# Kernel tuning notes

Measured on AMD Instinct MI355X. Metric: run time of the kernel, lower is better.

Reference implementation:

```python
import math
import jax, jax.numpy as jnp
import numpy as np

B, T, D = 2048, 50, 256
NEG = -100000.0

def setup_inputs() -> dict:
    key = jax.random.key(0)
    ks = jax.random.split(key, 9)
    return {
        "x": jax.random.normal(ks[0], (B, T, D), dtype=jnp.float32),
        "mask": jax.random.randint(ks[1], (B, T, 1), 0, 2, dtype=jnp.int32),
        "time_decay": jax.random.uniform(ks[2], (B, T, 1), dtype=jnp.float32),
        "Wq": jax.random.normal(ks[3], (D, D), dtype=jnp.float32) * (1.0 / math.sqrt(D)),
        "bq": jax.random.normal(ks[4], (D,), dtype=jnp.float32) * 0.01,
        "Wk": jax.random.normal(ks[5], (D, D), dtype=jnp.float32) * (1.0 / math.sqrt(D)),
        "bk": jax.random.normal(ks[6], (D,), dtype=jnp.float32) * 0.01,
        "Wv": jax.random.normal(ks[7], (D, D), dtype=jnp.float32) * (1.0 / math.sqrt(D)),
        "bv": jax.random.normal(ks[8], (D,), dtype=jnp.float32) * 0.01,
    }

def reference(x, mask, time_decay, Wq, bq, Wk, bk, Wv, bv):
    # PositionalEncoding.forward: elementwise multiply by time-decay (broadcast over d_model)
    x = x * time_decay  # [B,T,D]
    q = jnp.einsum('btd,ed->bte', x, Wq) + bq
    k = jnp.einsum('btd,ed->bte', x, Wk) + bk
    v = jnp.einsum('btd,ed->bte', x, Wv) + bv
    # unusual Q/K-side masking (masked_fill before the matmul)
    keep = mask != 0  # [B,T,1]
    q = jnp.where(keep, q, NEG)
    k = jnp.where(keep, k, NEG)
    score = jnp.einsum('btd,bsd->bts', q, k) / math.sqrt(D)  # [B,T,T]
    score = jax.nn.softmax(score, axis=-1)
    # dropout is identity in eval mode
    out = jnp.einsum('bts,bsd->btd', score, v)  # [B,T,D]
    return out[:, -1, :]  # [B,D]
```

## Files before the change

kernel.cpp:

```cpp
#include <hip/hip_runtime.h>


namespace {
constexpr int kB = 2048;
constexpr int kT = 50;
constexpr int kD = 256;
constexpr double kNeg = -100000.0;
constexpr int oM2 = 0;
constexpr int oWvp = 65536;
constexpr int oV0 = 131072;
constexpr int oC = 131328;
constexpr int oW1 = 131584;
constexpr int oW2 = 131840;
constexpr int oDbl = 132096;
}

__global__ __launch_bounds__(256) void precomp(
    const float* __restrict__ Wq, const float* __restrict__ bq,
    const float* __restrict__ Wk, const float* __restrict__ bk,
    const float* __restrict__ Wv, float* __restrict__ ws) {
  const int t = threadIdx.x;
  const int wave = t >> 6;
  const int lane = t & 63;
  const int blk = blockIdx.x;
  __shared__ float coefL[kD];
  __shared__ double red[3][4];

  if (blk < 256) {
    const int a = blk;
    coefL[t] = Wq[(size_t)t * kD + a];
    __syncthreads();
    const float* kcol = Wk + t;
    float pre[8];
#pragma unroll
    for (int k = 0; k < 8; ++k) pre[k] = kcol[(size_t)k * kD];
    float acc = 0.f;
    for (int j0 = 0; j0 < kD; j0 += 8) {
      float cur[8];
#pragma unroll
      for (int k = 0; k < 8; ++k) cur[k] = pre[k];
      const int nx = (j0 + 8 < kD) ? (j0 + 8) : 0;
#pragma unroll
      for (int k = 0; k < 8; ++k) pre[k] = kcol[(size_t)(nx + k) * kD];
#pragma unroll
      for (int k = 0; k < 8; ++k) acc += coefL[j0 + k] * cur[k];
    }
    ws[oM2 + (a >> 2) * 1024 + 4 * t + (a & 3)] = acc;
  } else if (blk < 258) {
    const float* W = (blk == 256) ? Wk : Wq;
    const float* coef = (blk == 256) ? bq : bk;
    coefL[t] = coef[t];
    __syncthreads();
    const float* col = W + t;
    float pre[8];
#pragma unroll
    for (int k = 0; k < 8; ++k) pre[k] = col[(size_t)k * kD];
    double a0 = 0.0, a1 = 0.0;
    for (int j0 = 0; j0 < kD; j0 += 8) {
      float cur[8];
#pragma unroll
      for (int k = 0; k < 8; ++k) cur[k] = pre[k];
      const int nx = (j0 + 8 < kD) ? (j0 + 8) : 0;
#pragma unroll
      for (int k = 0; k < 8; ++k) pre[k] = col[(size_t)(nx + k) * kD];
#pragma unroll
      for (int k = 0; k < 8; ++k) {
        const double w = (double)cur[k];
        a0 += (double)coefL[j0 + k] * w;
        a1 += w;
      }
    }
    if (blk == 256) {
      ws[oV0 + t] = (float)a0;
      ws[oC + t] = (float)a1;
    } else {
      ws[oW1 + t] = (float)a0;
      ws[oW2 + t] = (float)a1;
      double p0 = (double)bk[t];
      double p1 = (double)bq[t] * (double)bk[t];
      double p2 = (double)bq[t];
#pragma unroll
      for (int off = 32; off; off >>= 1) {
        p0 += __shfl_xor(p0, off);
        p1 += __shfl_xor(p1, off);
        p2 += __shfl_xor(p2, off);
      }
      if (lane == 0) {
        red[0][wave] = p0;
        red[1][wave] = p1;
        red[2][wave] = p2;
      }
      __syncthreads();
      if (t == 0) {
        double* dcw = (double*)(ws + oDbl);
        dcw[0] = red[0][0] + red[0][1] + red[0][2] + red[0][3];
        dcw[1] = red[1][0] + red[1][1] + red[1][2] + red[1][3];
        dcw[2] = red[2][0] + red[2][1] + red[2][2] + red[2][3];
      }
    }
  } else {
    const int d4b = (blk - 258) * 4;
    float4 in[4];
#pragma unroll
    for (int k = 0; k < 4; ++k)
      in[k] = *(const float4*)(Wv + (size_t)t * kD + 4 * (d4b + k));
    float4* Wvp = (float4*)(ws + oWvp);
#pragma unroll
    for (int k = 0; k < 4; ++k) Wvp[(size_t)(d4b + k) * kD + t] = in[k];
  }
}

__global__ __launch_bounds__(512, 4) void fused_main(
    const float* __restrict__ x, const int* __restrict__ mask,
    const float* __restrict__ td, const float* __restrict__ bv,
    const float* __restrict__ ws, float* __restrict__ out) {
  const int tid = threadIdx.x;
  const int lane = tid & 63;
  const int w = tid >> 6;
  const int b0 = blockIdx.x * 2;
  __shared__ __align__(16) float xsL[2][kD];
  __shared__ __align__(16) float uL[2][kD];
  __shared__ __align__(16) float yL[2][kD];
  __shared__ __align__(16) float scr[2][4][kD];
  __shared__ double mpart[2][4];
  __shared__ float lpart[2][4];
  __shared__ double dScal[2][2];

  const double* dc = (const double*)(ws + oDbl);
  const float4* M2v = (const float4*)(ws + oM2);
  const float4* Wvv = (const float4*)(ws + oWvp);

  const int ja = w >> 2;
  const int q = w & 3;
  const float mtdA = (lane < kT) ? td[(size_t)(b0 + ja) * kT + lane] : 0.f;
  const int mmkA = (lane < kT) ? mask[(size_t)(b0 + ja) * kT + lane] : 0;
  const float4 c4 = ((const float4*)(ws + oC))[lane];

  if (q == 0) {
    const int j = ja;
    const int b = b0 + j;
    const float tdl = __shfl(mtdA, kT - 1);
    const float4 a1 = ((const float4*)(ws + oW1))[lane];
    const float4 a2 = ((const float4*)(ws + oW2))[lane];
    const float4 xv =
        ((const float4*)(x + ((size_t)b * kT + kT - 1) * kD))[lane];
    double s1 = (double)xv.x * a1.x + (double)xv.y * a1.y +
                (double)xv.z * a1.z + (double)xv.w * a1.w;
    double s2 = (double)xv.x * a2.x + (double)xv.y * a2.y +
                (double)xv.z * a2.z + (double)xv.w * a2.w;
#pragma unroll
    for (int off = 32; off; off >>= 1) {
      s1 += __shfl_xor(s1, off);
      s2 += __shfl_xor(s2, off);
    }
    if (lane == 0) {
      dScal[j][0] = (double)tdl * s1 + dc[1];
      dScal[j][1] = (double)tdl * s2 + dc[2];
    }
    float4 xs;
    xs.x = xv.x * tdl; xs.y = xv.y * tdl;
    xs.z = xv.z * tdl; xs.w = xv.w * tdl;
    *(float4*)(&xsL[j][4 * lane]) = xs;
  }
  __syncthreads();

  {
    const int gU = w >> 1;
    const int kh = w & 1;
    const int col = 64 * gU + lane;
    const int kb = kh * 32;
    float4 A = M2v[(size_t)kb * 256 + col];
    float4 B = M2v[(size_t)(kb + 1) * 256 + col];
    float acc0 = 0.f, acc1 = 0.f;
    for (int k4 = kb; k4 < kb + 32; k4 += 2) {
      const float4 c0 = A, c1 = B;
      const int n0 = (k4 + 2 < kb + 32) ? k4 + 2 : kb;
      const int n1 = (k4 + 3 < kb + 32) ? k4 + 3 : kb + 1;
      A = M2v[(size_t)n0 * 256 + col];
      B = M2v[(size_t)n1 * 256 + col];
      const float4 x00 = *(const float4*)(&xsL[0][4 * k4]);
      const float4 x01 = *(const float4*)(&xsL[0][4 * (k4 + 1)]);
      const float4 x10 = *(const float4*)(&xsL[1][4 * k4]);
      const float4 x11 = *(const float4*)(&xsL[1][4 * (k4 + 1)]);
      acc0 += x00.x * c0.x + x00.y * c0.y + x00.z * c0.z + x00.w * c0.w +
              x01.x * c1.x + x01.y * c1.y + x01.z * c1.z + x01.w * c1.w;
      acc1 += x10.x * c0.x + x10.y * c0.y + x10.z * c0.z + x10.w * c0.w +
              x11.x * c1.x + x11.y * c1.y + x11.z * c1.z + x11.w * c1.w;
    }
    scr[kh][0][col] = acc0;
    scr[kh][1][col] = acc1;
  }
  __syncthreads();

  {
    const int mj = tid >> 8;
    const int mcol = tid & 255;
    uL[mj][mcol] = scr[0][mj][mcol] + scr[1][mj][mcol] + ws[oV0 + mcol];
  }
  __syncthreads();

  {
    const int j = ja;
    const int b = b0 + j;
    const float mtd = mtdA;
    const int mmk = mmkA;
    const int mqg = __shfl(mmk, kT - 1);
    const float4 u4 = *(const float4*)(&uL[j][4 * lane]);
    const float4 v4 = mqg ? u4 : c4;
    const double Qb = dScal[j][0];
    const double Cm = kNeg * dScal[j][1] * 0.0625;
    const double sbkd = dc[0];
    const double Cbb = 256.0 * 1.0e10 * 0.0625;
    const int sbeg = (q == 0) ? 0 : (q == 1) ? 13 : (q == 2) ? 26 : 38;
    const int send = (q == 0) ? 13 : (q == 1) ? 26 : (q == 2) ? 38 : 50;

    const float4* xrow = (const float4*)(x + (size_t)b * kT * kD);
    double m = -1.0e300;
    float l = 0.f;
    float4 y = {0.f, 0.f, 0.f, 0.f};

    const int i0 = (sbeg + 0 < kT) ? sbeg + 0 : kT - 1;
    const int i1 = (sbeg + 1 < kT) ? sbeg + 1 : kT - 1;
    const int i2 = (sbeg + 2 < kT) ? sbeg + 2 : kT - 1;
    const int i3 = (sbeg + 3 < kT) ? sbeg + 3 : kT - 1;
    float4 n0 = xrow[(size_t)i0 * 64 + lane];
    float4 n1 = xrow[(size_t)i1 * 64 + lane];
    float4 n2 = xrow[(size_t)i2 * 64 + lane];
    float4 n3 = xrow[(size_t)i3 * 64 + lane];
    for (int s = sbeg; s < send; s += 4) {
      const float4 r0 = n0, r1 = n1, r2 = n2, r3 = n3;
      {
        const int p0 = (s + 4 < kT) ? s + 4 : kT - 1;
        const int p1 = (s + 5 < kT) ? s + 5 : kT - 1;
        const int p2 = (s + 6 < kT) ? s + 6 : kT - 1;
        const int p3 = (s + 7 < kT) ? s + 7 : kT - 1;
        n0 = xrow[(size_t)p0 * 64 + lane];
        n1 = xrow[(size_t)p1 * 64 + lane];
        n2 = xrow[(size_t)p2 * 64 + lane];
        n3 = xrow[(size_t)p3 * 64 + lane];
      }
      const int s1i = s + 1, s2i = s + 2, s3i = s + 3;
      const int cc0 = s;
      const int cc1 = (s1i < kT) ? s1i : kT - 1;
      const int cc2 = (s2i < kT) ? s2i : kT - 1;
      const int cc3 = (s3i < kT) ? s3i : kT - 1;
      const float tv0 = __shfl(mtd, cc0);
      const float tv1 = __shfl(mtd, cc1);
      const float tv2 = __shfl(mtd, cc2);
      const float tv3 = __shfl(mtd, cc3);
      float4 a0, aa1, a2v, a3;
      a0.x = r0.x * tv0; a0.y = r0.y * tv0; a0.z = r0.z * tv0; a0.w = r0.w * tv0;
      aa1.x = r1.x * tv1; aa1.y = r1.y * tv1; aa1.z = r1.z * tv1; aa1.w = r1.w * tv1;
      a2v.x = r2.x * tv2; a2v.y = r2.y * tv2; a2v.z = r2.z * tv2; a2v.w = r2.w * tv2;
      a3.x = r3.x * tv3; a3.y = r3.y * tv3; a3.z = r3.z * tv3; a3.w = r3.w * tv3;
      float p0 = a0.x * v4.x + a0.y * v4.y + a0.z * v4.z + a0.w * v4.w;
      float p1 = aa1.x * v4.x + aa1.y * v4.y + aa1.z * v4.z + aa1.w * v4.w;
      float p2 = a2v.x * v4.x + a2v.y * v4.y + a2v.z * v4.z + a2v.w * v4.w;
      float p3 = a3.x * v4.x + a3.y * v4.y + a3.z * v4.z + a3.w * v4.w;
#pragma unroll
      for (int off = 32; off; off >>= 1) {
        p0 += __shfl_xor(p0, off);
        p1 += __shfl_xor(p1, off);
        p2 += __shfl_xor(p2, off);
        p3 += __shfl_xor(p3, off);
      }
      const int ms0 = __shfl(mmk, cc0);
      const int ms1 = __shfl(mmk, cc1);
      const int ms2 = __shfl(mmk, cc2);
      const int ms3 = __shfl(mmk, cc3);
      double sc0, sc1, sc2, sc3;
      if (mqg) {
        sc0 = ms0 ? ((double)p0 + Qb) * 0.0625 : Cm;
        sc1 = ms1 ? ((double)p1 + Qb) * 0.0625 : Cm;
        sc2 = ms2 ? ((double)p2 + Qb) * 0.0625 : Cm;
        sc3 = ms3 ? ((double)p3 + Qb) * 0.0625 : Cm;
      } else {
        sc0 = ms0 ? kNeg * ((double)p0 + sbkd) * 0.0625 : Cbb;
        sc1 = ms1 ? kNeg * ((double)p1 + sbkd) * 0.0625 : Cbb;
        sc2 = ms2 ? kNeg * ((double)p2 + sbkd) * 0.0625 : Cbb;
        sc3 = ms3 ? kNeg * ((double)p3 + sbkd) * 0.0625 : Cbb;
      }
      if (s1i >= send) sc1 = -1.0e300;
      if (s2i >= send) sc2 = -1.0e300;
      if (s3i >= send) sc3 = -1.0e300;
      double mnew = m;
      if (sc0 > mnew) mnew = sc0;
      if (sc1 > mnew) mnew = sc1;
      if (sc2 > mnew) mnew = sc2;
      if (sc3 > mnew) mnew = sc3;
      const float al = __expf((float)(m - mnew));
      const float e0 = __expf((float)(sc0 - mnew));
      const float e1 = __expf((float)(sc1 - mnew));
      const float e2 = __expf((float)(sc2 - mnew));
      const float e3 = __expf((float)(sc3 - mnew));
      m = mnew;
      l = l * al + e0 + e1 + e2 + e3;
      y.x = y.x * al + e0 * a0.x + e1 * aa1.x + e2 * a2v.x + e3 * a3.x;
      y.y = y.y * al + e0 * a0.y + e1 * aa1.y + e2 * a2v.y + e3 * a3.y;
      y.z = y.z * al + e0 * a0.z + e1 * aa1.z + e2 * a2v.z + e3 * a3.z;
      y.w = y.w * al + e0 * a0.w + e1 * aa1.w + e2 * a2v.w + e3 * a3.w;
    }
    if (lane == 0) {
      mpart[j][q] = m;
      lpart[j][q] = l;
    }
    *(float4*)(&scr[j][q][4 * lane]) = y;
  }
  __syncthreads();

  {
    const int mj = tid >> 8;
    const int mcol = tid & 255;
    double M = mpart[mj][0];
    if (mpart[mj][1] > M) M = mpart[mj][1];
    if (mpart[mj][2] > M) M = mpart[mj][2];
    if (mpart[mj][3] > M) M = mpart[mj][3];
    const float e0 = __expf((float)(mpart[mj][0] - M));
    const float e1 = __expf((float)(mpart[mj][1] - M));
    const float e2 = __expf((float)(mpart[mj][2] - M));
    const float e3 = __expf((float)(mpart[mj][3] - M));
    const float l = lpart[mj][0] * e0 + lpart[mj][1] * e1 +
                    lpart[mj][2] * e2 + lpart[mj][3] * e3;
    const float inv = 1.0f / l;
    const float yv = (scr[mj][0][mcol] * e0 + scr[mj][1][mcol] * e1 +
                      scr[mj][2][mcol] * e2 + scr[mj][3][mcol] * e3) *
                     inv;
    __syncthreads();
    yL[mj][mcol] = yv;
  }
  __syncthreads();

  {
    const int gU = w >> 1;
    const int kh = w & 1;
    const int col = 64 * gU + lane;
    const int kb = kh * 32;
    float4 A = Wvv[(size_t)kb * 256 + col];
    float4 B = Wvv[(size_t)(kb + 1) * 256 + col];
    float acc0 = 0.f, acc1 = 0.f;
    for (int k4 = kb; k4 < kb + 32; k4 += 2) {
      const float4 c0 = A, c1 = B;
      const int n0 = (k4 + 2 < kb + 32) ? k4 + 2 : kb;
      const int n1 = (k4 + 3 < kb + 32) ? k4 + 3 : kb + 1;
      A = Wvv[(size_t)n0 * 256 + col];
      B = Wvv[(size_t)n1 * 256 + col];
      const float4 y00 = *(const float4*)(&yL[0][4 * k4]);
      const float4 y01 = *(const float4*)(&yL[0][4 * (k4 + 1)]);
      const float4 y10 = *(const float4*)(&yL[1][4 * k4]);
      const float4 y11 = *(const float4*)(&yL[1][4 * (k4 + 1)]);
      acc0 += y00.x * c0.x + y00.y * c0.y + y00.z * c0.z + y00.w * c0.w +
              y01.x * c1.x + y01.y * c1.y + y01.z * c1.z + y01.w * c1.w;
      acc1 += y10.x * c0.x + y10.y * c0.y + y10.z * c0.z + y10.w * c0.w +
              y11.x * c1.x + y11.y * c1.y + y11.z * c1.z + y11.w * c1.w;
    }
    scr[kh][0][col] = acc0;
    scr[kh][1][col] = acc1;
  }
  __syncthreads();

  {
    const int mj = tid >> 8;
    const int mcol = tid & 255;
    out[(size_t)(b0 + mj) * kD + mcol] =
        scr[0][mj][mcol] + scr[1][mj][mcol] + bv[mcol];
  }
}

extern "C" void kernel_launch(void* const* d_in, const int* in_sizes, int n_in,
                              void* d_out, int out_size, void* d_ws,
                              size_t ws_size, hipStream_t stream) {
  const float* x = (const float*)d_in[0];
  const int* mask = (const int*)d_in[1];
  const float* td = (const float*)d_in[2];
  const float* Wq = (const float*)d_in[3];
  const float* bq = (const float*)d_in[4];
  const float* Wk = (const float*)d_in[5];
  const float* bk = (const float*)d_in[6];
  const float* Wv = (const float*)d_in[7];
  const float* bv = (const float*)d_in[8];
  float* ws = (float*)d_ws;
  float* out = (float*)d_out;
  (void)in_sizes; (void)n_in; (void)out_size; (void)ws_size;

  hipLaunchKernelGGL(precomp, dim3(274), dim3(256), 0, stream, Wq, bq, Wk, bk,
                     Wv, ws);
  hipLaunchKernelGGL(fused_main, dim3(kB / 2), dim3(512), 0, stream, x, mask,
                     td, bv, (const float*)ws, out);
}
```

Measured before the change: 210.9 us.

## Process four batch rows per block to reuse weight loads across more rows

Each block now handles four batch elements instead of two, so every M2/Wv matrix-vector pass loads each weight column once and applies it to four rows, halving weight traffic per row. To fit, the attention sweep over the sequence is split into two halves per row instead of four, and the merge step combines two partials. The weight prefetch is deepened to four float4s, and the occupancy hint in launch bounds is dropped. The cost is less parallelism per row in the attention loop, more registers, and half as many blocks.

```diff
diff --git a/kernel.cpp b/kernel.cpp
--- a/kernel.cpp
+++ b/kernel.cpp
@@ -5,6 +5,7 @@
 constexpr int kB = 2048;
 constexpr int kT = 50;
 constexpr int kD = 256;
+constexpr int kBB = 4;
 constexpr double kNeg = -100000.0;
 constexpr int oM2 = 0;
 constexpr int oWvp = 65536;
@@ -110,36 +111,36 @@
   }
 }
 
-__global__ __launch_bounds__(512, 4) void fused_main(
+__global__ __launch_bounds__(512) void fused_main(
     const float* __restrict__ x, const int* __restrict__ mask,
     const float* __restrict__ td, const float* __restrict__ bv,
     const float* __restrict__ ws, float* __restrict__ out) {
   const int tid = threadIdx.x;
   const int lane = tid & 63;
   const int w = tid >> 6;
-  const int b0 = blockIdx.x * 2;
-  __shared__ __align__(16) float xsL[2][kD];
-  __shared__ __align__(16) float uL[2][kD];
-  __shared__ __align__(16) float yL[2][kD];
-  __shared__ __align__(16) float scr[2][4][kD];
-  __shared__ double mpart[2][4];
-  __shared__ float lpart[2][4];
-  __shared__ double dScal[2][2];
+  const int b0 = blockIdx.x * kBB;
+  __shared__ __align__(16) float xsL[kBB][kD];
+  __shared__ __align__(16) float uL[kBB][kD];
+  __shared__ __align__(16) float yL[kBB][kD];
+  __shared__ __align__(16) float scr[2][kBB][kD];
+  __shared__ double mpart[kBB][2];
+  __shared__ float lpart[kBB][2];
+  __shared__ double dScal[kBB][2];
 
   const double* dc = (const double*)(ws + oDbl);
   const float4* M2v = (const float4*)(ws + oM2);
   const float4* Wvv = (const float4*)(ws + oWvp);
 
-  const int ja = w >> 2;
-  const int q = w & 3;
+  const int ja = w >> 1;
+  const int h = w & 1;
   const float mtdA = (lane < kT) ? td[(size_t)(b0 + ja) * kT + lane] : 0.f;
   const int mmkA = (lane < kT) ? mask[(size_t)(b0 + ja) * kT + lane] : 0;
   const float4 c4 = ((const float4*)(ws + oC))[lane];
 
-  if (q == 0) {
-    const int j = ja;
+  if (w < kBB) {
+    const int j = w;
     const int b = b0 + j;
-    const float tdl = __shfl(mtdA, kT - 1);
+    const float tdl = td[(size_t)b * kT + kT - 1];
     const float4 a1 = ((const float4*)(ws + oW1))[lane];
     const float4 a2 = ((const float4*)(ws + oW2))[lane];
     const float4 xv =
@@ -165,37 +166,44 @@
   __syncthreads();
 
   {
-    const int gU = w >> 1;
-    const int kh = w & 1;
+    const int gU = w & 3;
+    const int kh = w >> 2;
     const int col = 64 * gU + lane;
     const int kb = kh * 32;
-    float4 A = M2v[(size_t)kb * 256 + col];
+    float4 A = M2v[(size_t)(kb + 0) * 256 + col];
     float4 B = M2v[(size_t)(kb + 1) * 256 + col];
-    float acc0 = 0.f, acc1 = 0.f;
+    float4 C = M2v[(size_t)(kb + 2) * 256 + col];
+    float4 D = M2v[(size_t)(kb + 3) * 256 + col];
+    float acc[kBB] = {0.f, 0.f, 0.f, 0.f};
     for (int k4 = kb; k4 < kb + 32; k4 += 2) {
       const float4 c0 = A, c1 = B;
-      const int n0 = (k4 + 2 < kb + 32) ? k4 + 2 : kb;
-      const int n1 = (k4 + 3 < kb + 32) ? k4 + 3 : kb + 1;
-      A = M2v[(size_t)n0 * 256 + col];
-      B = M2v[(size_t)n1 * 256 + col];
-      const float4 x00 = *(const float4*)(&xsL[0][4 * k4]);
-      const float4 x01 = *(const float4*)(&xsL[0][4 * (k4 + 1)]);
-      const float4 x10 = *(const float4*)(&xsL[1][4 * k4]);
-      const float4 x11 = *(const float4*)(&xsL[1][4 * (k4 + 1)]);
-      acc0 += x00.x * c0.x + x00.y * c0.y + x00.z * c0.z + x00.w * c0.w +
-              x01.x * c1.x + x01.y * c1.y + x01.z * c1.z + x01.w * c1.w;
-      acc1 += x10.x * c0.x + x10.y * c0.y + x10.z * c0.z + x10.w * c0.w +
-              x11.x * c1.x + x11.y * c1.y + x11.z * c1.z + x11.w * c1.w;
-    }
-    scr[kh][0][col] = acc0;
-    scr[kh][1][col] = acc1;
-  }
-  __syncthreads();
-
-  {
-    const int mj = tid >> 8;
-    const int mcol = tid & 255;
-    uL[mj][mcol] = scr[0][mj][mcol] + scr[1][mj][mcol] + ws[oV0 + mcol];
+      A = C;
+      B = D;
+      const int n0 = (k4 + 4 < kb + 32) ? k4 + 4 : kb;
+      const int n1 = (k4 + 5 < kb + 32) ? k4 + 5 : kb;
+      C = M2v[(size_t)n0 * 256 + col];
+      D = M2v[(size_t)n1 * 256 + col];
+#pragma unroll
+      for (int jb = 0; jb < kBB; ++jb) {
+        const float4 x0 = *(const float4*)(&xsL[jb][4 * k4]);
+        const float4 x1 = *(const float4*)(&xsL[jb][4 * (k4 + 1)]);
+        acc[jb] += x0.x * c0.x + x0.y * c0.y + x0.z * c0.z + x0.w * c0.w +
+                   x1.x * c1.x + x1.y * c1.y + x1.z * c1.z + x1.w * c1.w;
+      }
+    }
+#pragma unroll
+    for (int jb = 0; jb < kBB; ++jb) scr[kh][jb][col] = acc[jb];
+  }
+  __syncthreads();
+
+  {
+#pragma unroll
+    for (int rr = 0; rr < 2; ++rr) {
+      const int idx = tid + rr * 512;
+      const int mj = idx >> 8;
+      const int mcol = idx & 255;
+      uL[mj][mcol] = scr[0][mj][mcol] + scr[1][mj][mcol] + ws[oV0 + mcol];
+    }
   }
   __syncthreads();
 
@@ -211,22 +219,18 @@
     const double Cm = kNeg * dScal[j][1] * 0.0625;
     const double sbkd = dc[0];
     const double Cbb = 256.0 * 1.0e10 * 0.0625;
-    const int sbeg = (q == 0) ? 0 : (q == 1) ? 13 : (q == 2) ? 26 : 38;
-    const int send = (q == 0) ? 13 : (q == 1) ? 26 : (q == 2) ? 38 : 50;
+    const int sbeg = h ? 24 : 0;
+    const int send = h ? 50 : 24;
 
     const float4* xrow = (const float4*)(x + (size_t)b * kT * kD);
     double m = -1.0e300;
     float l = 0.f;
     float4 y = {0.f, 0.f, 0.f, 0.f};
 
-    const int i0 = (sbeg + 0 < kT) ? sbeg + 0 : kT - 1;
-    const int i1 = (sbeg + 1 < kT) ? sbeg + 1 : kT - 1;
-    const int i2 = (sbeg + 2 < kT) ? sbeg + 2 : kT - 1;
-    const int i3 = (sbeg + 3 < kT) ? sbeg + 3 : kT - 1;
-    float4 n0 = xrow[(size_t)i0 * 64 + lane];
-    float4 n1 = xrow[(size_t)i1 * 64 + lane];
-    float4 n2 = xrow[(size_t)i2 * 64 + lane];
-    float4 n3 = xrow[(size_t)i3 * 64 + lane];
+    float4 n0 = xrow[(size_t)(sbeg + 0) * 64 + lane];
+    float4 n1 = xrow[(size_t)(sbeg + 1) * 64 + lane];
+    float4 n2 = xrow[(size_t)(sbeg + 2) * 64 + lane];
+    float4 n3 = xrow[(size_t)(sbeg + 3) * 64 + lane];
     for (int s = sbeg; s < send; s += 4) {
       const float4 r0 = n0, r1 = n1, r2 = n2, r3 = n3;
       {
@@ -301,68 +305,76 @@
       y.w = y.w * al + e0 * a0.w + e1 * aa1.w + e2 * a2v.w + e3 * a3.w;
     }
     if (lane == 0) {
-      mpart[j][q] = m;
-      lpart[j][q] = l;
-    }
-    *(float4*)(&scr[j][q][4 * lane]) = y;
-  }
-  __syncthreads();
-
-  {
-    const int mj = tid >> 8;
-    const int mcol = tid & 255;
-    double M = mpart[mj][0];
-    if (mpart[mj][1] > M) M = mpart[mj][1];
-    if (mpart[mj][2] > M) M = mpart[mj][2];
-    if (mpart[mj][3] > M) M = mpart[mj][3];
-    const float e0 = __expf((float)(mpart[mj][0] - M));
-    const float e1 = __expf((float)(mpart[mj][1] - M));
-    const float e2 = __expf((float)(mpart[mj][2] - M));
-    const float e3 = __expf((float)(mpart[mj][3] - M));
-    const float l = lpart[mj][0] * e0 + lpart[mj][1] * e1 +
-                    lpart[mj][2] * e2 + lpart[mj][3] * e3;
-    const float inv = 1.0f / l;
-    const float yv = (scr[mj][0][mcol] * e0 + scr[mj][1][mcol] * e1 +
-                      scr[mj][2][mcol] * e2 + scr[mj][3][mcol] * e3) *
-                     inv;
+      mpart[j][h] = m;
+      lpart[j][h] = l;
+    }
+    *(float4*)(&scr[h][j][4 * lane]) = y;
+  }
+  __syncthreads();
+
+  {
+    float yv[2];
+    int mjA[2], mcolA[2];
+#pragma unroll
+    for (int rr = 0; rr < 2; ++rr) {
+      const int idx = tid + rr * 512;
+      const int mj = idx >> 8;
+      const int mcol = idx & 255;
+      const double m0 = mpart[mj][0], m1 = mpart[mj][1];
+      const double M = (m0 > m1) ? m0 : m1;
+      const float e0 = __expf((float)(m0 - M));
+      const float e1 = __expf((float)(m1 - M));
+      const float l = lpart[mj][0] * e0 + lpart[mj][1] * e1;
+      yv[rr] = (scr[0][mj][mcol] * e0 + scr[1][mj][mcol] * e1) * (1.0f / l);
+      mjA[rr] = mj;
+      mcolA[rr] = mcol;
+    }
     __syncthreads();
-    yL[mj][mcol] = yv;
-  }
-  __syncthreads();
-
-  {
-    const int gU = w >> 1;
-    const int kh = w & 1;
+    yL[mjA[0]][mcolA[0]] = yv[0];
+    yL[mjA[1]][mcolA[1]] = yv[1];
+  }
+  __syncthreads();
+
+  {
+    const int gU = w & 3;
+    const int kh = w >> 2;
     const int col = 64 * gU + lane;
     const int kb = kh * 32;
-    float4 A = Wvv[(size_t)kb * 256 + col];
+    float4 A = Wvv[(size_t)(kb + 0) * 256 + col];
     float4 B = Wvv[(size_t)(kb + 1) * 256 + col];
-    float acc0 = 0.f, acc1 = 0.f;
+    float4 C = Wvv[(size_t)(kb + 2) * 256 + col];
+    float4 D = Wvv[(size_t)(kb + 3) * 256 + col];
+    float acc[kBB] = {0.f, 0.f, 0.f, 0.f};
     for (int k4 = kb; k4 < kb + 32; k4 += 2) {
       const float4 c0 = A, c1 = B;
-      const int n0 = (k4 + 2 < kb + 32) ? k4 + 2 : kb;
-      const int n1 = (k4 + 3 < kb + 32) ? k4 + 3 : kb + 1;
-      A = Wvv[(size_t)n0 * 256 + col];
-      B = Wvv[(size_t)n1 * 256 + col];
-      const float4 y00 = *(const float4*)(&yL[0][4 * k4]);
-      const float4 y01 = *(const float4*)(&yL[0][4 * (k4 + 1)]);
-      const float4 y10 = *(const float4*)(&yL[1][4 * k4]);
-      const float4 y11 = *(const float4*)(&yL[1][4 * (k4 + 1)]);
-      acc0 += y00.x * c0.x + y00.y * c0.y + y00.z * c0.z + y00.w * c0.w +
-              y01.x * c1.x + y01.y * c1.y + y01.z * c1.z + y01.w * c1.w;
-      acc1 += y10.x * c0.x + y10.y * c0.y + y10.z * c0.z + y10.w * c0.w +
-              y11.x * c1.x + y11.y * c1.y + y11.z * c1.z + y11.w * c1.w;
-    }
-    scr[kh][0][col] = acc0;
-    scr[kh][1][col] = acc1;
-  }
-  __syncthreads();
-
-  {
-    const int mj = tid >> 8;
-    const int mcol = tid & 255;
-    out[(size_t)(b0 + mj) * kD + mcol] =
-        scr[0][mj][mcol] + scr[1][mj][mcol] + bv[mcol];
+      A = C;
+      B = D;
+      const int n0 = (k4 + 4 < kb + 32) ? k4 + 4 : kb;
+      const int n1 = (k4 + 5 < kb + 32) ? k4 + 5 : kb;
+      C = Wvv[(size_t)n0 * 256 + col];
+      D = Wvv[(size_t)n1 * 256 + col];
+#pragma unroll
+      for (int jb = 0; jb < kBB; ++jb) {
+        const float4 y0 = *(const float4*)(&yL[jb][4 * k4]);
+        const float4 y1 = *(const float4*)(&yL[jb][4 * (k4 + 1)]);
+        acc[jb] += y0.x * c0.x + y0.y * c0.y + y0.z * c0.z + y0.w * c0.w +
+                   y1.x * c1.x + y1.y * c1.y + y1.z * c1.z + y1.w * c1.w;
+      }
+    }
+#pragma unroll
+    for (int jb = 0; jb < kBB; ++jb) scr[kh][jb][col] = acc[jb];
+  }
+  __syncthreads();
+
+  {
+#pragma unroll
+    for (int rr = 0; rr < 2; ++rr) {
+      const int idx = tid + rr * 512;
+      const int mj = idx >> 8;
+      const int mcol = idx & 255;
+      out[(size_t)(b0 + mj) * kD + mcol] =
+          scr[0][mj][mcol] + scr[1][mj][mcol] + bv[mcol];
+    }
   }
 }
 
@@ -384,6 +396,6 @@
 
   hipLaunchKernelGGL(precomp, dim3(274), dim3(256), 0, stream, Wq, bq, Wk, bk,
                      Wv, ws);
-  hipLaunchKernelGGL(fused_main, dim3(kB / 2), dim3(512), 0, stream, x, mask,
+  hipLaunchKernelGGL(fused_main, dim3(kB / kBB), dim3(512), 0, stream, x, mask,
                      td, bv, (const float*)ws, out);
 }
```

Result: faster. 202.0 us (-4.2%).
